# Kernel tuning notes

Hardware: AMD Instinct MI355X
Metric: run time of the kernel (lower is better)

The kernel has to match this reference:

```python
import jax, jax.numpy as jnp
import numpy as np

ALPHA = 0.25
GAMMA = 2.0
W_CLASS = 2.0
W_BBOX = 5.0
W_GIOU = 2.0
EPS = 1e-8

B, N, C, M = 128, 900, 91, 100


def cxcywh_to_xyxy(b):
    cx, cy, w, h = jnp.split(b, 4, axis=-1)
    return jnp.concatenate([cx - 0.5 * w, cy - 0.5 * h, cx + 0.5 * w, cy + 0.5 * h], axis=-1)


def generalized_box_iou(a, b):
    # a: [B, N, 4], b: [B, M, 4], both xyxy -> giou [B, N, M]
    area_a = (a[..., 2] - a[..., 0]) * (a[..., 3] - a[..., 1])  # [B, N]
    area_b = (b[..., 2] - b[..., 0]) * (b[..., 3] - b[..., 1])  # [B, M]
    lt = jnp.maximum(a[:, :, None, :2], b[:, None, :, :2])      # [B, N, M, 2]
    rb = jnp.minimum(a[:, :, None, 2:], b[:, None, :, 2:])
    wh = jnp.clip(rb - lt, 0.0)
    inter = wh[..., 0] * wh[..., 1]                             # [B, N, M]
    union = area_a[:, :, None] + area_b[:, None, :] - inter
    iou = inter / union
    lt_e = jnp.minimum(a[:, :, None, :2], b[:, None, :, :2])
    rb_e = jnp.maximum(a[:, :, None, 2:], b[:, None, :, 2:])
    wh_e = jnp.clip(rb_e - lt_e, 0.0)
    area_e = wh_e[..., 0] * wh_e[..., 1]
    return iou - (area_e - union) / area_e


def setup_inputs() -> dict:
    key = jax.random.key(0)
    k1, k2, k3, k4 = jax.random.split(key, 4)
    pred_logits = jax.random.normal(k1, (B, N, C), dtype=jnp.float32)
    pred_boxes = jax.random.uniform(k2, (B, N, 4), dtype=jnp.float32)   # cxcywh in [0,1)
    tgt_labels = jax.random.randint(k3, (B, M), 0, C, dtype=jnp.int64 if jax.config.jax_enable_x64 else jnp.int32)
    tgt_boxes = jax.random.uniform(k4, (B, M, 4), dtype=jnp.float32)    # cxcywh in [0,1)
    return {"pred_logits": pred_logits, "pred_boxes": pred_boxes,
            "tgt_labels": tgt_labels, "tgt_boxes": tgt_boxes}


def reference(pred_logits, pred_boxes, tgt_labels, tgt_boxes):
    """Batched Hungarian-matcher cost matrix [B, N, M].

    Faithful to HungarianMatcher.forward's cost construction:
      cost = w_class * (pos_focal - neg_focal)[.., tgt_label]
           + w_bbox  * cdist_L1(pred_boxes, tgt_boxes)
           + w_giou  * (-GIoU(pred_xyxy, tgt_xyxy))
    The scipy linear_sum_assignment step is a host-side combinatorial solve
    on this matrix and is not part of the tensor math being baselined.
    """
    s = jax.nn.sigmoid(pred_logits)                              # [B, N, C]
    neg_cost = (1.0 - ALPHA) * s ** GAMMA * (-jnp.log(1.0 - s + EPS))
    pos_cost = ALPHA * (1.0 - s) ** GAMMA * (-jnp.log(s + EPS))
    cls_cost_full = pos_cost - neg_cost                          # [B, N, C]
    # gather per-target class costs -> [B, N, M]
    cost_class = jnp.take_along_axis(
        cls_cost_full, tgt_labels[:, None, :].astype(jnp.int32), axis=2)
    # L1 cdist over the 4 box coords -> [B, N, M]
    cost_bbox = jnp.sum(jnp.abs(pred_boxes[:, :, None, :] - tgt_boxes[:, None, :, :]), axis=-1)
    cost_giou = -generalized_box_iou(cxcywh_to_xyxy(pred_boxes), cxcywh_to_xyxy(tgt_boxes))
    return W_CLASS * cost_class + W_BBOX * cost_bbox + W_GIOU * cost_giou
```

## Files before the change

### kernel.cpp

```cpp
#include <hip/hip_runtime.h>

constexpr int B = 128, N = 900, C = 91, M = 100;
constexpr float ALPHA = 0.25f;
constexpr float W_CLASS = 2.0f;
constexpr float W_BBOX = 5.0f;
constexpr float W_GIOU = 2.0f;

constexpr int NBX  = 15;
constexpr int ROWS = N / NBX;
constexpr int BLK  = 256;
constexpr int MQ   = M / 4;
constexpr int NGRP = 10;
constexpr int KIT  = ROWS / NGRP;

typedef float f32x4 __attribute__((ext_vector_type(4)));

__global__ __launch_bounds__(BLK) void hungarian_cost_kernel(
    const float* __restrict__ logits,
    const float* __restrict__ pboxes,
    const int*   __restrict__ tlabels,
    const float* __restrict__ tboxes,
    float* __restrict__ out)
{
    const int b   = blockIdx.y;
    const int n0  = blockIdx.x * ROWS;
    const int tid = threadIdx.x;

    const int mq   = tid % MQ;
    const int rgrp = tid / MQ;
    if (rgrp >= NGRP) return;

    const float*  lbase = logits + ((size_t)b * N + n0) * C;
    const float4* pbp   = reinterpret_cast<const float4*>(pboxes) + (size_t)b * N + n0;
    f32x4*        outq  = reinterpret_cast<f32x4*>(out) + ((size_t)b * N + n0) * MQ;

    const int4 l4 = reinterpret_cast<const int4*>(tlabels + (size_t)b * M)[mq];
    int labj[4] = {l4.x, l4.y, l4.z, l4.w};

    float4 pv[KIT];
    float  xsv[KIT][4];
    #pragma unroll
    for (int k = 0; k < KIT; ++k) {
        const int row = rgrp + NGRP * k;
        pv[k] = pbp[row];
        const float* lr = lbase + row * C;
        #pragma unroll
        for (int j = 0; j < 4; ++j) xsv[k][j] = lr[labj[j]];
    }

    float tcx[4], tcy[4], twd[4], tht[4];
    float tx0[4], ty0[4], tx1[4], ty1[4], tar[4];
    {
        const float4* tbp = reinterpret_cast<const float4*>(tboxes) + (size_t)b * M;
        #pragma unroll
        for (int j = 0; j < 4; ++j) {
            const float4 t = tbp[mq * 4 + j];
            tcx[j] = t.x; tcy[j] = t.y; twd[j] = t.z; tht[j] = t.w;
            tx0[j] = t.x - 0.5f * t.z;  ty0[j] = t.y - 0.5f * t.w;
            tx1[j] = t.x + 0.5f * t.z;  ty1[j] = t.y + 0.5f * t.w;
            tar[j] = (tx1[j] - tx0[j]) * (ty1[j] - ty0[j]);
        }
    }

    #pragma unroll
    for (int k = 0; k < KIT; ++k) {
        const int row = rgrp + NGRP * k;
        const float4 p = pv[k];

        const float px0 = p.x - 0.5f * p.z, py0 = p.y - 0.5f * p.w;
        const float px1 = p.x + 0.5f * p.z, py1 = p.y + 0.5f * p.w;
        const float parea = (px1 - px0) * (py1 - py0);

        f32x4 res;
        #pragma unroll
        for (int j = 0; j < 4; ++j) {
            const float x    = xsv[k][j];
            const float e    = __expf(-x);
            const float onep = 1.0f + e;
            const float s    = __builtin_amdgcn_rcpf(onep);
            const float om   = e * s;
            const float L    = __logf(onep);
            const float ccls = W_CLASS * (ALPHA * om * om * L
                                        - (1.0f - ALPHA) * s * s * (x + L));

            const float l1 = fabsf(p.x - tcx[j]) + fabsf(p.y - tcy[j]) +
                             fabsf(p.z - twd[j]) + fabsf(p.w - tht[j]);

            const float iw = fmaxf(fminf(px1, tx1[j]) - fmaxf(px0, tx0[j]), 0.0f);
            const float ih = fmaxf(fminf(py1, ty1[j]) - fmaxf(py0, ty0[j]), 0.0f);
            const float inter = iw * ih;
            const float uni   = parea + tar[j] - inter;

            const float ew = fmaxf(px1, tx1[j]) - fminf(px0, tx0[j]);
            const float eh = fmaxf(py1, ty1[j]) - fminf(py0, ty0[j]);
            const float earea = ew * eh;

            const float num  = inter * earea - uni * (earea - uni);
            const float rcpD = __builtin_amdgcn_rcpf(uni * earea);

            res[j] = ccls + W_BBOX * l1 - W_GIOU * (num * rcpD);
        }

        __builtin_nontemporal_store(res, &outq[(size_t)row * MQ + mq]);
    }
}

extern "C" void kernel_launch(void* const* d_in, const int* in_sizes, int n_in,
                              void* d_out, int out_size, void* d_ws, size_t ws_size,
                              hipStream_t stream) {
    const float* logits  = (const float*)d_in[0];
    const float* pboxes  = (const float*)d_in[1];
    const int*   tlabels = (const int*)d_in[2];
    const float* tboxes  = (const float*)d_in[3];
    float* out = (float*)d_out;

    dim3 grid(NBX, B);
    dim3 block(BLK);
    hipLaunchKernelGGL(hungarian_cost_kernel, grid, block, 0, stream,
                       logits, pboxes, tlabels, tboxes, out);
}
```

Before: 27.30 us.

## Double-buffer per-row loads and simplify class and L1 cost arithmetic

Instead of loading all six rows' box and logit values up front, the loop now prefetches only the next row while computing the current one, with a scheduling barrier between the two. This is meant to lower register pressure and overlap gather latency with compute. The focal class cost is folded algebraically into fewer multiplies. The L1 term is computed from the xyxy corners, so the cxcywh target copies no longer need registers. The risk is fewer loads in flight at once, and the sched_barrier may limit how the compiler interleaves instructions.

Measured after the change: 26.94 us. About the same (-1.3%).

```diff
diff --git a/kernel.cpp b/kernel.cpp
--- a/kernel.cpp
+++ b/kernel.cpp
@@ -1,8 +1,6 @@
 #include <hip/hip_runtime.h>
 
 constexpr int B = 128, N = 900, C = 91, M = 100;
-constexpr float ALPHA = 0.25f;
-constexpr float W_CLASS = 2.0f;
 constexpr float W_BBOX = 5.0f;
 constexpr float W_GIOU = 2.0f;
 
@@ -35,38 +33,44 @@
     f32x4*        outq  = reinterpret_cast<f32x4*>(out) + ((size_t)b * N + n0) * MQ;
 
     const int4 l4 = reinterpret_cast<const int4*>(tlabels + (size_t)b * M)[mq];
-    int labj[4] = {l4.x, l4.y, l4.z, l4.w};
+    const int labj[4] = {l4.x, l4.y, l4.z, l4.w};
 
-    float4 pv[KIT];
-    float  xsv[KIT][4];
-    #pragma unroll
-    for (int k = 0; k < KIT; ++k) {
-        const int row = rgrp + NGRP * k;
-        pv[k] = pbp[row];
-        const float* lr = lbase + row * C;
-        #pragma unroll
-        for (int j = 0; j < 4; ++j) xsv[k][j] = lr[labj[j]];
-    }
-
-    float tcx[4], tcy[4], twd[4], tht[4];
     float tx0[4], ty0[4], tx1[4], ty1[4], tar[4];
     {
         const float4* tbp = reinterpret_cast<const float4*>(tboxes) + (size_t)b * M;
         #pragma unroll
         for (int j = 0; j < 4; ++j) {
             const float4 t = tbp[mq * 4 + j];
-            tcx[j] = t.x; tcy[j] = t.y; twd[j] = t.z; tht[j] = t.w;
             tx0[j] = t.x - 0.5f * t.z;  ty0[j] = t.y - 0.5f * t.w;
             tx1[j] = t.x + 0.5f * t.z;  ty1[j] = t.y + 0.5f * t.w;
             tar[j] = (tx1[j] - tx0[j]) * (ty1[j] - ty0[j]);
         }
     }
 
+    float4 pA, pB;
+    float  xA[4], xB[4];
+    {
+        const int row0 = rgrp;
+        pA = pbp[row0];
+        const float* lr = lbase + row0 * C;
+        #pragma unroll
+        for (int j = 0; j < 4; ++j) xA[j] = lr[labj[j]];
+    }
+
     #pragma unroll
     for (int k = 0; k < KIT; ++k) {
         const int row = rgrp + NGRP * k;
-        const float4 p = pv[k];
 
+        if (k + 1 < KIT) {
+            const int rown = row + NGRP;
+            pB = pbp[rown];
+            const float* lr = lbase + rown * C;
+            #pragma unroll
+            for (int j = 0; j < 4; ++j) xB[j] = lr[labj[j]];
+        }
+        __builtin_amdgcn_sched_barrier(0);
+
+        const float4 p = pA;
         const float px0 = p.x - 0.5f * p.z, py0 = p.y - 0.5f * p.w;
         const float px1 = p.x + 0.5f * p.z, py1 = p.y + 0.5f * p.w;
         const float parea = (px1 - px0) * (py1 - py0);
@@ -74,17 +78,19 @@
         f32x4 res;
         #pragma unroll
         for (int j = 0; j < 4; ++j) {
-            const float x    = xsv[k][j];
+            const float x    = xA[j];
             const float e    = __expf(-x);
             const float onep = 1.0f + e;
             const float s    = __builtin_amdgcn_rcpf(onep);
-            const float om   = e * s;
             const float L    = __logf(onep);
-            const float ccls = W_CLASS * (ALPHA * om * om * L
-                                        - (1.0f - ALPHA) * s * s * (x + L));
+            const float s2   = s * s;
+            const float coef = (0.5f - s) - s2;
+            const float ccls = L * coef - 1.5f * s2 * x;
 
-            const float l1 = fabsf(p.x - tcx[j]) + fabsf(p.y - tcy[j]) +
-                             fabsf(p.z - twd[j]) + fabsf(p.w - tht[j]);
+            const float dx0 = px0 - tx0[j], dx1 = px1 - tx1[j];
+            const float dy0 = py0 - ty0[j], dy1 = py1 - ty1[j];
+            const float l1 = 0.5f * (fabsf(dx0 + dx1) + fabsf(dy0 + dy1))
+                           + fabsf(dx1 - dx0) + fabsf(dy1 - dy0);
 
             const float iw = fmaxf(fminf(px1, tx1[j]) - fmaxf(px0, tx0[j]), 0.0f);
             const float ih = fmaxf(fminf(py1, ty1[j]) - fmaxf(py0, ty0[j]), 0.0f);
@@ -102,6 +108,10 @@
         }
 
         __builtin_nontemporal_store(res, &outq[(size_t)row * MQ + mq]);
+
+        pA = pB;
+        #pragma unroll
+        for (int j = 0; j < 4; ++j) xA[j] = xB[j];
     }
 }
 
```
